# Kernel optimization log

Hardware: AMD Instinct MI355X
Metric: run time of the kernel (lower is better)

Reference implementation:

```python
import jax, jax.numpy as jnp
import numpy as np

D_MODEL = 1024

def setup_inputs() -> dict:
    key = jax.random.key(0)
    ks = jax.random.split(key, 7)
    B, T, D = 4, 4096, D_MODEL
    s = 1.0 / np.sqrt(D)
    return {
        "x": jax.random.normal(ks[0], (B, T, D), dtype=jnp.float32),
        "Wq": jax.random.normal(ks[1], (D, D), dtype=jnp.float32) * s,
        "bq": jax.random.normal(ks[2], (D,), dtype=jnp.float32) * 0.01,
        "Wk": jax.random.normal(ks[3], (D, D), dtype=jnp.float32) * s,
        "bk": jax.random.normal(ks[4], (D,), dtype=jnp.float32) * 0.01,
        "Wv": jax.random.normal(ks[5], (D, D), dtype=jnp.float32) * s,
        "bv": jax.random.normal(ks[6], (D,), dtype=jnp.float32) * 0.01,
    }

def reference(x, Wq, bq, Wk, bk, Wv, bv):
    # x: [B, T, D]; Linear weights stored [out, in] like torch -> x @ W.T + b
    D = x.shape[-1]
    T = x.shape[1]
    scale = jnp.sqrt(jnp.asarray(D, dtype=x.dtype))
    Q = jnp.einsum('btd,ed->bte', x, Wq) + bq
    K = jnp.einsum('btd,ed->bte', x, Wk) + bk
    V = jnp.einsum('btd,ed->bte', x, Wv) + bv
    scores = jnp.einsum('bqd,bkd->bqk', Q, K) / scale  # [B, T, T]
    causal = jnp.tril(jnp.ones((T, T), dtype=bool))    # True = keep (q >= k)
    neg_inf = jnp.asarray(-jnp.inf, dtype=scores.dtype)
    scores = jnp.where(causal, scores, neg_inf)
    probs = jax.nn.softmax(scores, axis=-1)
    return jnp.einsum('bqk,bkd->bqd', probs, V)
```

## Files before the change

### kernel.cpp

```cpp
#include <hip/hip_runtime.h>
#include <hip/hip_bf16.h>
#include <math.h>


typedef __bf16 bf16;
typedef __bf16 bf16x8 __attribute__((ext_vector_type(8)));
typedef float  f32x4  __attribute__((ext_vector_type(4)));

#define LOG2E 1.4426950408889634f

static constexpr size_t OFF_XB   = 0;
static constexpr size_t OFF_WQB  = 33554432;
static constexpr size_t OFF_WKB  = 35651584;
static constexpr size_t OFF_WVB  = 37748736;
static constexpr size_t OFF_Q    = 39845888;
static constexpr size_t OFF_K    = 73400320;
static constexpr size_t OFF_VT   = 106954752;
static constexpr size_t OFF_S    = 140509184;
static constexpr size_t OFF_PSUM = 209715200;
static constexpr size_t OFF_LINV = 211812352;

typedef __attribute__((address_space(1))) void gvoid_t;
typedef __attribute__((address_space(3))) void lvoid_t;

__device__ __forceinline__ void gload16(const void* g, void* l) {
  __builtin_amdgcn_global_load_lds((gvoid_t*)g, (lvoid_t*)l, 16, 0, 0);
}

struct Ctx { int tid, lane, quad, col16, wr, wc, wcol; };
__device__ __forceinline__ Ctx mk_ctx() {
  Ctx c; c.tid = (int)threadIdx.x; c.lane = c.tid & 63;
  int w = c.tid >> 6;
  c.quad = c.lane >> 4; c.col16 = c.lane & 15;
  c.wr = (w >> 1) * 64; c.wc = (w & 1) * 64; c.wcol = w & 1;
  return c;
}

__device__ __forceinline__ void stage_tile(const bf16* g, long ld, bf16* s, int tid) {
  int lane = tid & 63, w = tid >> 6;
  const bf16* gp = g + (long)(lane >> 2) * ld + (long)(lane & 3) * 8;
  long step = 16 * ld;
  gload16(gp + (long)(2 * w) * step,     s + (2 * w) * 512);
  gload16(gp + (long)(2 * w + 1) * step, s + (2 * w + 1) * 512);
}

__device__ __forceinline__ void mfma_step(const bf16* sA, const bf16* sB,
                                          const Ctx& c, f32x4 acc[4][4]) {
  bf16x8 a[4], b[4];
#pragma unroll
  for (int i = 0; i < 4; ++i) {
    a[i] = *(const bf16x8*)(sA + ((c.wr + i * 16 + c.col16) * 32 + c.quad * 8));
    b[i] = *(const bf16x8*)(sB + ((c.wc + i * 16 + c.col16) * 32 + c.quad * 8));
  }
#pragma unroll
  for (int i = 0; i < 4; ++i)
#pragma unroll
    for (int j = 0; j < 4; ++j)
      acc[i][j] = __builtin_amdgcn_mfma_f32_16x16x32_bf16(a[i], b[j], acc[i][j], 0, 0, 0);
}

__device__ __forceinline__ void zero_acc(f32x4 acc[4][4]) {
  f32x4 z = {0.f, 0.f, 0.f, 0.f};
#pragma unroll
  for (int i = 0; i < 4; ++i)
#pragma unroll
    for (int j = 0; j < 4; ++j) acc[i][j] = z;
}

__device__ __forceinline__ int tridec(int i) {
  int qt = (int)((sqrtf(8.0f * (float)i + 1.0f) - 1.0f) * 0.5f);
  while ((qt + 1) * (qt + 2) / 2 <= i) ++qt;
  while (qt * (qt + 1) / 2 > i) --qt;
  return qt;
}


__global__ __launch_bounds__(256) void cvt_all(const float* __restrict__ x,
                                               const float* __restrict__ Wq,
                                               const float* __restrict__ Wk,
                                               const float* __restrict__ Wv,
                                               bf16* __restrict__ xb,
                                               bf16* __restrict__ wqb,
                                               bf16* __restrict__ wkb,
                                               bf16* __restrict__ wvb) {
  int b = (int)blockIdx.x;
  const float* in; bf16* out; long base;
  if (b < 8192)      { in = x;  out = xb;  base = (long)b * 2048; }
  else if (b < 8704) { in = Wq; out = wqb; base = (long)(b - 8192) * 2048; }
  else if (b < 9216) { in = Wk; out = wkb; base = (long)(b - 8704) * 2048; }
  else               { in = Wv; out = wvb; base = (long)(b - 9216) * 2048; }
  long i = base + (long)threadIdx.x * 8;
  float4 f0 = *(const float4*)(in + i);
  float4 f1 = *(const float4*)(in + i + 4);
  bf16x8 h;
  h[0] = (bf16)f0.x; h[1] = (bf16)f0.y; h[2] = (bf16)f0.z; h[3] = (bf16)f0.w;
  h[4] = (bf16)f1.x; h[5] = (bf16)f1.y; h[6] = (bf16)f1.z; h[7] = (bf16)f1.w;
  *(bf16x8*)(out + i) = h;
}

__global__ __launch_bounds__(256) void qk_gemm(const bf16* __restrict__ X,
                                               const bf16* __restrict__ Wq,
                                               const bf16* __restrict__ Wk,
                                               const float* __restrict__ bq,
                                               const float* __restrict__ bk,
                                               bf16* __restrict__ Q,
                                               bf16* __restrict__ K) {
  __shared__ __align__(16) bf16 sA[128 * 32], sB[128 * 32];
  Ctx c = mk_ctx();
  const bf16*  W    = blockIdx.z ? Wk : Wq;
  const float* bias = blockIdx.z ? bk : bq;
  bf16*        out  = blockIdx.z ? K : Q;
  long r0 = (long)blockIdx.y * 128, c0 = (long)blockIdx.x * 128;
  f32x4 acc[4][4]; zero_acc(acc);
  for (int k = 0; k < 1024; k += 32) {
    stage_tile(X + r0 * 1024 + k, 1024, sA, c.tid);
    stage_tile(W + c0 * 1024 + k, 1024, sB, c.tid);
    __syncthreads();
    mfma_step(sA, sB, c, acc);
    __syncthreads();
  }
#pragma unroll
  for (int j = 0; j < 4; ++j) {
    int col = c.wc + j * 16 + c.col16;
    float bb = bias[c0 + col];
#pragma unroll
    for (int i = 0; i < 4; ++i) {
      int rowb = c.wr + i * 16 + c.quad * 4;
#pragma unroll
      for (int r = 0; r < 4; ++r)
        out[(r0 + rowb + r) * 1024 + c0 + col] = (bf16)(acc[i][j][r] + bb);
    }
  }
}

__global__ __launch_bounds__(256) void vt_gemm(const bf16* __restrict__ X,
                                               const bf16* __restrict__ Wv,
                                               const float* __restrict__ bv,
                                               bf16* __restrict__ Vt) {
  __shared__ __align__(16) bf16 sA[128 * 32], sB[128 * 32];
  Ctx c = mk_ctx();
  int z = blockIdx.z;
  long r0 = (long)blockIdx.y * 128;
  long c0 = (long)blockIdx.x * 128;
  const bf16* Ab = Wv + r0 * 1024;
  const bf16* Bb = X + (long)z * 4194304 + c0 * 1024;
  f32x4 acc[4][4]; zero_acc(acc);
  for (int k = 0; k < 1024; k += 32) {
    stage_tile(Ab + k, 1024, sA, c.tid);
    stage_tile(Bb + k, 1024, sB, c.tid);
    __syncthreads();
    mfma_step(sA, sB, c, acc);
    __syncthreads();
  }
  bf16* out = Vt + (long)z * 4194304;
#pragma unroll
  for (int i = 0; i < 4; ++i) {
    int rowb = c.wr + i * 16 + c.quad * 4;
    float bb[4];
#pragma unroll
    for (int r = 0; r < 4; ++r) bb[r] = bv[r0 + rowb + r];
#pragma unroll
    for (int j = 0; j < 4; ++j) {
      int col = c.wc + j * 16 + c.col16;
#pragma unroll
      for (int r = 0; r < 4; ++r)
        out[(r0 + rowb + r) * 4096 + c0 + col] = (bf16)(acc[i][j][r] + bb[r]);
    }
  }
}

__global__ __launch_bounds__(256) void s_gemm(const bf16* __restrict__ Q,
                                              const bf16* __restrict__ K,
                                              bf16* __restrict__ S,
                                              float* __restrict__ psum) {
  __shared__ __align__(16) bf16 sA[128 * 32], sB[128 * 32];
  __shared__ float sred[2][128];
  Ctx c = mk_ctx();
  int ti = blockIdx.x, z = blockIdx.z;
  int qt = tridec(ti);
  int kt = ti - qt * (qt + 1) / 2;
  long q0 = (long)qt * 128, k0 = (long)kt * 128;
  const bf16* Ab = Q + (long)z * 4194304 + q0 * 1024;
  const bf16* Bb = K + (long)z * 4194304 + k0 * 1024;
  f32x4 acc[4][4]; zero_acc(acc);
  for (int k = 0; k < 1024; k += 32) {
    stage_tile(Ab + k, 1024, sA, c.tid);
    stage_tile(Bb + k, 1024, sB, c.tid);
    __syncthreads();
    mfma_step(sA, sB, c, acc);
    __syncthreads();
  }
  bf16* st = S + ((long)z * 528 + ti) * 16384;
  const bool diag = (qt == kt);
  float rs[4][4];
#pragma unroll
  for (int i = 0; i < 4; ++i) {
#pragma unroll
    for (int r = 0; r < 4; ++r) {
      int row_l = c.wr + i * 16 + c.quad * 4 + r;
      float s = 0.f;
#pragma unroll
      for (int j = 0; j < 4; ++j) {
        int col_l = c.wc + j * 16 + c.col16;
        float p = exp2f(acc[i][j][r] * (0.03125f * LOG2E));
        if (diag && col_l > row_l) p = 0.0f;
        bf16 h = (bf16)p;
        st[row_l * 128 + col_l] = h;
        s += (float)h;
      }
      rs[i][r] = s;
    }
  }
#pragma unroll
  for (int i = 0; i < 4; ++i)
#pragma unroll
    for (int r = 0; r < 4; ++r)
#pragma unroll
      for (int m = 1; m <= 8; m <<= 1)
        rs[i][r] += __shfl_xor(rs[i][r], m);
  if (c.col16 == 0) {
#pragma unroll
    for (int i = 0; i < 4; ++i)
#pragma unroll
      for (int r = 0; r < 4; ++r)
        sred[c.wcol][c.wr + i * 16 + c.quad * 4 + r] = rs[i][r];
  }
  __syncthreads();
  if (c.tid < 128)
    psum[((long)z * 4096 + q0 + c.tid) * 32 + kt] = sred[0][c.tid] + sred[1][c.tid];
}

__global__ __launch_bounds__(256) void inv_sums(const float* __restrict__ psum,
                                                float* __restrict__ linv) {
  long i = (long)blockIdx.x * 256 + threadIdx.x;
  int q = (int)(i & 4095);
  int nt = (q >> 7) + 1;
  const float* ps = psum + i * 32;
  float l = 0.f;
  for (int t = 0; t < nt; ++t) l += ps[t];
  linv[i] = 1.0f / l;
}

__global__ __launch_bounds__(256) void o_gemm(const bf16* __restrict__ S,
                                              const bf16* __restrict__ Vt,
                                              const float* __restrict__ linv,
                                              float* __restrict__ out) {
  __shared__ __align__(16) bf16 sA[128 * 32], sB[128 * 32];
  Ctx c = mk_ctx();
  int b = (int)blockIdx.x;
  int z = b & 3, et = (b >> 2) & 7, qt = b >> 5;
  long q0 = (long)qt * 128, e0 = (long)et * 128;
  const bf16* Bb = Vt + (long)z * 4194304 + e0 * 4096;
  long tribase = ((long)z * 528 + (long)qt * (qt + 1) / 2) * 16384;
  f32x4 acc[4][4]; zero_acc(acc);
  int kend = (qt + 1) * 128;
  for (int k = 0; k < kend; k += 32) {
    const bf16* Ab = S + tribase + (long)(k >> 7) * 16384 + (k & 127);
    stage_tile(Ab, 128, sA, c.tid);
    stage_tile(Bb + k, 4096, sB, c.tid);
    __syncthreads();
    mfma_step(sA, sB, c, acc);
    __syncthreads();
  }
  long zq = (long)z * 4096 + q0;
#pragma unroll
  for (int i = 0; i < 4; ++i) {
    int rowb = c.wr + i * 16 + c.quad * 4;
    float li[4];
#pragma unroll
    for (int r = 0; r < 4; ++r) li[r] = linv[zq + rowb + r];
#pragma unroll
    for (int j = 0; j < 4; ++j) {
      int col = c.wc + j * 16 + c.col16;
#pragma unroll
      for (int r = 0; r < 4; ++r)
        out[(zq + rowb + r) * 1024 + e0 + col] = acc[i][j][r] * li[r];
    }
  }
}

extern "C" void kernel_launch(void* const* d_in, const int* in_sizes, int n_in,
                              void* d_out, int out_size, void* d_ws, size_t ws_size,
                              hipStream_t stream) {
  (void)in_sizes; (void)n_in; (void)out_size; (void)ws_size;
  const float* x  = (const float*)d_in[0];
  const float* Wq = (const float*)d_in[1];
  const float* bq = (const float*)d_in[2];
  const float* Wk = (const float*)d_in[3];
  const float* bk = (const float*)d_in[4];
  const float* Wv = (const float*)d_in[5];
  const float* bv = (const float*)d_in[6];

  char* ws = (char*)d_ws;
  bf16*  xb   = (bf16*)(ws + OFF_XB);
  bf16*  wqb  = (bf16*)(ws + OFF_WQB);
  bf16*  wkb  = (bf16*)(ws + OFF_WKB);
  bf16*  wvb  = (bf16*)(ws + OFF_WVB);
  bf16*  Qb   = (bf16*)(ws + OFF_Q);
  bf16*  Kb   = (bf16*)(ws + OFF_K);
  bf16*  Vtb  = (bf16*)(ws + OFF_VT);
  bf16*  Sb   = (bf16*)(ws + OFF_S);
  float* psum = (float*)(ws + OFF_PSUM);
  float* linv = (float*)(ws + OFF_LINV);

  cvt_all<<<9728, 256, 0, stream>>>(x, Wq, Wk, Wv, xb, wqb, wkb, wvb);

  qk_gemm<<<dim3(8, 128, 2), 256, 0, stream>>>(xb, wqb, wkb, bq, bk, Qb, Kb);
  vt_gemm<<<dim3(32, 8, 4), 256, 0, stream>>>(xb, wvb, bv, Vtb);
  s_gemm<<<dim3(528, 1, 4), 256, 0, stream>>>(Qb, Kb, Sb, psum);
  inv_sums<<<64, 256, 0, stream>>>(psum, linv);
  o_gemm<<<1024, 256, 0, stream>>>(Sb, Vtb, linv, (float*)d_out);
}
```

Measured before the change: 523.7 us.

## Merge QK and Vt projections into one launch, use K=64 steps, balance o_gemm order

```diff
diff --git a/kernel.cpp b/kernel.cpp
--- a/kernel.cpp
+++ b/kernel.cpp
@@ -98,73 +98,80 @@
   *(bf16x8*)(out + i) = h;
 }
 
-__global__ __launch_bounds__(256) void qk_gemm(const bf16* __restrict__ X,
-                                               const bf16* __restrict__ Wq,
-                                               const bf16* __restrict__ Wk,
-                                               const float* __restrict__ bq,
-                                               const float* __restrict__ bk,
-                                               bf16* __restrict__ Q,
-                                               bf16* __restrict__ K) {
-  __shared__ __align__(16) bf16 sA[128 * 32], sB[128 * 32];
+__global__ __launch_bounds__(256) void qkv_gemm(const bf16* __restrict__ X,
+                                                const bf16* __restrict__ Wq,
+                                                const bf16* __restrict__ Wk,
+                                                const bf16* __restrict__ Wv,
+                                                const float* __restrict__ bq,
+                                                const float* __restrict__ bk,
+                                                const float* __restrict__ bv,
+                                                bf16* __restrict__ Q,
+                                                bf16* __restrict__ K,
+                                                bf16* __restrict__ Vt) {
+  __shared__ __align__(16) bf16 sA[2][128 * 32], sB[2][128 * 32];
   Ctx c = mk_ctx();
-  const bf16*  W    = blockIdx.z ? Wk : Wq;
-  const float* bias = blockIdx.z ? bk : bq;
-  bf16*        out  = blockIdx.z ? K : Q;
-  long r0 = (long)blockIdx.y * 128, c0 = (long)blockIdx.x * 128;
+  int b = (int)blockIdx.x;
+  const bf16 *Ag, *Bg;
+  bool is_vt = (b >= 2048);
+  long r0, c0;
+  if (!is_vt) {
+    int isK = (b >> 10) & 1, rem = b & 1023;
+    c0 = (long)(rem & 7) * 128;
+    r0 = (long)(rem >> 3) * 128;
+    Ag = X + r0 * 1024;
+    Bg = (isK ? Wk : Wq) + c0 * 1024;
+  } else {
+    int vb = b - 2048;
+    int z = vb & 3, e = (vb >> 2) & 7, t = vb >> 5;
+    r0 = (long)e * 128;
+    c0 = (long)t * 128;
+    Ag = Wv + r0 * 1024;
+    Bg = X + (long)z * 4194304 + c0 * 1024;
+  }
   f32x4 acc[4][4]; zero_acc(acc);
-  for (int k = 0; k < 1024; k += 32) {
-    stage_tile(X + r0 * 1024 + k, 1024, sA, c.tid);
-    stage_tile(W + c0 * 1024 + k, 1024, sB, c.tid);
-    __syncthreads();
-    mfma_step(sA, sB, c, acc);
-    __syncthreads();
-  }
-#pragma unroll
-  for (int j = 0; j < 4; ++j) {
-    int col = c.wc + j * 16 + c.col16;
-    float bb = bias[c0 + col];
+  for (int k = 0; k < 1024; k += 64) {
+    stage_tile(Ag + k,      1024, sA[0], c.tid);
+    stage_tile(Ag + k + 32, 1024, sA[1], c.tid);
+    stage_tile(Bg + k,      1024, sB[0], c.tid);
+    stage_tile(Bg + k + 32, 1024, sB[1], c.tid);
+    __syncthreads();
+    mfma_step(sA[0], sB[0], c, acc);
+    mfma_step(sA[1], sB[1], c, acc);
+    __syncthreads();
+  }
+  if (!is_vt) {
+    int isK = (b >> 10) & 1;
+    const float* bias = isK ? bk : bq;
+    bf16* out = isK ? K : Q;
+#pragma unroll
+    for (int j = 0; j < 4; ++j) {
+      int col = c.wc + j * 16 + c.col16;
+      float bb = bias[c0 + col];
+#pragma unroll
+      for (int i = 0; i < 4; ++i) {
+        int rowb = c.wr + i * 16 + c.quad * 4;
+#pragma unroll
+        for (int r = 0; r < 4; ++r)
+          out[(r0 + rowb + r) * 1024 + c0 + col] = (bf16)(acc[i][j][r] + bb);
+      }
+    }
+  } else {
+    int vb = b - 2048;
+    int z = vb & 3;
+    bf16* out = Vt + (long)z * 4194304;
 #pragma unroll
     for (int i = 0; i < 4; ++i) {
       int rowb = c.wr + i * 16 + c.quad * 4;
-#pragma unroll
-      for (int r = 0; r < 4; ++r)
-        out[(r0 + rowb + r) * 1024 + c0 + col] = (bf16)(acc[i][j][r] + bb);
-    }
-  }
-}
-
-__global__ __launch_bounds__(256) void vt_gemm(const bf16* __restrict__ X,
-                                               const bf16* __restrict__ Wv,
-                                               const float* __restrict__ bv,
-                                               bf16* __restrict__ Vt) {
-  __shared__ __align__(16) bf16 sA[128 * 32], sB[128 * 32];
-  Ctx c = mk_ctx();
-  int z = blockIdx.z;
-  long r0 = (long)blockIdx.y * 128;
-  long c0 = (long)blockIdx.x * 128;
-  const bf16* Ab = Wv + r0 * 1024;
-  const bf16* Bb = X + (long)z * 4194304 + c0 * 1024;
-  f32x4 acc[4][4]; zero_acc(acc);
-  for (int k = 0; k < 1024; k += 32) {
-    stage_tile(Ab + k, 1024, sA, c.tid);
-    stage_tile(Bb + k, 1024, sB, c.tid);
-    __syncthreads();
-    mfma_step(sA, sB, c, acc);
-    __syncthreads();
-  }
-  bf16* out = Vt + (long)z * 4194304;
-#pragma unroll
-  for (int i = 0; i < 4; ++i) {
-    int rowb = c.wr + i * 16 + c.quad * 4;
-    float bb[4];
-#pragma unroll
-    for (int r = 0; r < 4; ++r) bb[r] = bv[r0 + rowb + r];
-#pragma unroll
-    for (int j = 0; j < 4; ++j) {
-      int col = c.wc + j * 16 + c.col16;
-#pragma unroll
-      for (int r = 0; r < 4; ++r)
-        out[(r0 + rowb + r) * 4096 + c0 + col] = (bf16)(acc[i][j][r] + bb[r]);
+      float bb[4];
+#pragma unroll
+      for (int r = 0; r < 4; ++r) bb[r] = bv[r0 + rowb + r];
+#pragma unroll
+      for (int j = 0; j < 4; ++j) {
+        int col = c.wc + j * 16 + c.col16;
+#pragma unroll
+        for (int r = 0; r < 4; ++r)
+          out[(r0 + rowb + r) * 4096 + c0 + col] = (bf16)(acc[i][j][r] + bb[r]);
+      }
     }
   }
 }
@@ -173,7 +180,7 @@
                                               const bf16* __restrict__ K,
                                               bf16* __restrict__ S,
                                               float* __restrict__ psum) {
-  __shared__ __align__(16) bf16 sA[128 * 32], sB[128 * 32];
+  __shared__ __align__(16) bf16 sA[2][128 * 32], sB[2][128 * 32];
   __shared__ float sred[2][128];
   Ctx c = mk_ctx();
   int ti = blockIdx.x, z = blockIdx.z;
@@ -183,11 +190,14 @@
   const bf16* Ab = Q + (long)z * 4194304 + q0 * 1024;
   const bf16* Bb = K + (long)z * 4194304 + k0 * 1024;
   f32x4 acc[4][4]; zero_acc(acc);
-  for (int k = 0; k < 1024; k += 32) {
-    stage_tile(Ab + k, 1024, sA, c.tid);
-    stage_tile(Bb + k, 1024, sB, c.tid);
-    __syncthreads();
-    mfma_step(sA, sB, c, acc);
+  for (int k = 0; k < 1024; k += 64) {
+    stage_tile(Ab + k,      1024, sA[0], c.tid);
+    stage_tile(Ab + k + 32, 1024, sA[1], c.tid);
+    stage_tile(Bb + k,      1024, sB[0], c.tid);
+    stage_tile(Bb + k + 32, 1024, sB[1], c.tid);
+    __syncthreads();
+    mfma_step(sA[0], sB[0], c, acc);
+    mfma_step(sA[1], sB[1], c, acc);
     __syncthreads();
   }
   bf16* st = S + ((long)z * 528 + ti) * 16384;
@@ -245,21 +255,26 @@
                                               const bf16* __restrict__ Vt,
                                               const float* __restrict__ linv,
                                               float* __restrict__ out) {
-  __shared__ __align__(16) bf16 sA[128 * 32], sB[128 * 32];
+  __shared__ __align__(16) bf16 sA[2][128 * 32], sB[2][128 * 32];
   Ctx c = mk_ctx();
   int b = (int)blockIdx.x;
-  int z = b & 3, et = (b >> 2) & 7, qt = b >> 5;
+  int z = b & 3, et = (b >> 2) & 7, q0i = (b >> 5) & 7, gen = b >> 8;
+  int qt = (gen == 0) ? q0i : (gen == 1) ? 15 - q0i
+         : (gen == 2) ? 16 + q0i : 31 - q0i;
   long q0 = (long)qt * 128, e0 = (long)et * 128;
   const bf16* Bb = Vt + (long)z * 4194304 + e0 * 4096;
   long tribase = ((long)z * 528 + (long)qt * (qt + 1) / 2) * 16384;
   f32x4 acc[4][4]; zero_acc(acc);
   int kend = (qt + 1) * 128;
-  for (int k = 0; k < kend; k += 32) {
+  for (int k = 0; k < kend; k += 64) {
     const bf16* Ab = S + tribase + (long)(k >> 7) * 16384 + (k & 127);
-    stage_tile(Ab, 128, sA, c.tid);
-    stage_tile(Bb + k, 4096, sB, c.tid);
-    __syncthreads();
-    mfma_step(sA, sB, c, acc);
+    stage_tile(Ab,      128, sA[0], c.tid);
+    stage_tile(Ab + 32, 128, sA[1], c.tid);
+    stage_tile(Bb + k,      4096, sB[0], c.tid);
+    stage_tile(Bb + k + 32, 4096, sB[1], c.tid);
+    __syncthreads();
+    mfma_step(sA[0], sB[0], c, acc);
+    mfma_step(sA[1], sB[1], c, acc);
     __syncthreads();
   }
   long zq = (long)z * 4096 + q0;
@@ -304,9 +319,7 @@
   float* linv = (float*)(ws + OFF_LINV);
 
   cvt_all<<<9728, 256, 0, stream>>>(x, Wq, Wk, Wv, xb, wqb, wkb, wvb);
-
-  qk_gemm<<<dim3(8, 128, 2), 256, 0, stream>>>(xb, wqb, wkb, bq, bk, Qb, Kb);
-  vt_gemm<<<dim3(32, 8, 4), 256, 0, stream>>>(xb, wvb, bv, Vtb);
+  qkv_gemm<<<3072, 256, 0, stream>>>(xb, wqb, wkb, wvb, bq, bk, bv, Qb, Kb, Vtb);
   s_gemm<<<dim3(528, 1, 4), 256, 0, stream>>>(Qb, Kb, Sb, psum);
   inv_sums<<<64, 256, 0, stream>>>(psum, linv);
   o_gemm<<<1024, 256, 0, stream>>>(Sb, Vtb, linv, (float*)d_out);
```

Measured after the change: 504.0 us. -3.8%, faster.
